# Optimization experiments

Hardware: AMD Instinct MI355X
Metric: run time of the kernel (lower is better)

The kernel has to match this reference:

```python
import jax, jax.numpy as jnp
import numpy as np

B, A, C, M, N = 8, 49104, 20, 32, 16


def _make_boxes(key, shape):
    # valid boxes: x1<x2, y1<y2, in a ~1024px image
    k1, k2 = jax.random.split(key)
    xy = jax.random.uniform(k1, shape[:-1] + (2,)) * 900.0
    wh = jax.random.uniform(k2, shape[:-1] + (2,)) * 120.0 + 8.0
    return jnp.concatenate([xy, xy + wh], axis=-1).astype(jnp.float32)


def setup_inputs() -> dict:
    key = jax.random.key(0)
    ks = jax.random.split(key, 8)
    classifications = jax.random.uniform(ks[0], (B, A, C), dtype=jnp.float32)
    regressions = jax.random.normal(ks[1], (B, A, 4), dtype=jnp.float32)
    anchors = _make_boxes(ks[2], (1, A, 4))
    ema_classifications = jax.random.uniform(ks[3], (B, A, C), dtype=jnp.float32)
    ema_classes = jax.random.randint(ks[4], (B, M), 0, C).astype(jnp.float32)
    ema_bboxes = _make_boxes(ks[5], (B, M, 4))
    ema_counts = jax.random.randint(ks[6], (B,), 0, M + 1).astype(jnp.int32)
    ann_boxes = _make_boxes(ks[7], (B, N, 4))
    ann_cls = jax.random.randint(jax.random.fold_in(key, 99), (B, N), -1, C).astype(jnp.float32)
    annotations = jnp.concatenate([ann_boxes, ann_cls[..., None]], axis=-1)
    return {
        'classifications': classifications,
        'regressions': regressions,
        'anchors': anchors,
        'ema_classifications': ema_classifications,
        'ema_classes': ema_classes,
        'ema_bboxes': ema_bboxes,
        'ema_counts': ema_counts,
        'annotations': annotations,
    }


def _consistency_loss(classifications, regressions, anchors, ema_classifications,
                      ema_bboxes, ema_classes, ema_counts, annotations):
    a0, a1, gamma = 0.05, 0.95, 2.0
    eps = 1e-4
    Bs, As, Cs = classifications.shape
    Ms = ema_classes.shape[1]

    anchor = anchors[0]                        # [A,4]
    aw = anchor[:, 2] - anchor[:, 0]
    ah = anchor[:, 3] - anchor[:, 1]
    acx = anchor[:, 0] + 0.5 * aw
    acy = anchor[:, 1] + 0.5 * ah

    # ragged filtering: keep ema preds whose class appears in annotations[j,:,4]
    valid = jnp.arange(Ms)[None, :] < ema_counts[:, None]                    # [B,M]
    member = (ema_classes[:, :, None] == annotations[:, None, :, 4]).any(-1)  # [B,M]
    keep = valid & member
    has = keep.any(axis=1)                                                   # [B]

    # IoU between anchors [A,4] and kept ema boxes [B,M,4] -> [B,A,M]
    b = ema_bboxes
    iw = jnp.minimum(anchor[None, :, None, 2], b[:, None, :, 2]) - \
         jnp.maximum(anchor[None, :, None, 0], b[:, None, :, 0])
    ih = jnp.minimum(anchor[None, :, None, 3], b[:, None, :, 3]) - \
         jnp.maximum(anchor[None, :, None, 1], b[:, None, :, 1])
    iw = jnp.clip(iw, 0.0)
    ih = jnp.clip(ih, 0.0)
    area_a = (aw * ah)[None, :, None]
    area_b = ((b[:, :, 2] - b[:, :, 0]) * (b[:, :, 3] - b[:, :, 1]))[:, None, :]
    inter = iw * ih
    iou = inter / jnp.clip(area_a + area_b - inter, 1e-8)
    iou = jnp.where(keep[:, None, :], iou, -1.0)  # mask filtered/padded boxes

    iou_max = iou.max(axis=-1)                 # [B,A]
    iou_arg = iou.argmax(axis=-1)              # [B,A]

    pos = (iou_max >= 0.5) & has[:, None]                                   # [B,A]
    assigned = ((iou_max < 0.4) | (iou_max >= 0.5)) & has[:, None]          # [B,A]
    npos = pos.sum(axis=-1).astype(jnp.float32)                             # [B]

    # ---- classification consistency (focal-weighted BCE) ----
    cls = jnp.clip(classifications, eps, 1.0 - eps)
    ecls = jnp.clip(ema_classifications, eps, 1.0 - eps)
    # bug-faithful: original uses full-batch unclamped ema_classifications for
    # alpha_factor, broadcasting [B,A,C] against per-sample [A,C] terms and
    # summing everything; by linearity that equals multiplying by the batch-sum.
    alpha_sum = (a0 + ema_classifications * (a1 - a0)).sum(axis=0)          # [A,C]
    bce = -(ecls * jnp.log(cls) + (1.0 - ecls) * jnp.log(1.0 - cls))
    focal = jnp.abs(ecls - cls) ** gamma
    per = alpha_sum[None] * focal * bce                                     # [B,A,C]
    cls_loss = (per * assigned[:, :, None]).sum(axis=(1, 2)) / jnp.maximum(npos, 1.0)

    ab = jnp.take_along_axis(ema_bboxes, iou_arg[:, :, None], axis=1)       # [B,A,4]
    gw = ab[..., 2] - ab[..., 0]
    gh = ab[..., 3] - ab[..., 1]
    gcx = ab[..., 0] + 0.5 * gw
    gcy = ab[..., 1] + 0.5 * gh
    gw = jnp.clip(gw, 1.0)
    gh = jnp.clip(gh, 1.0)
    dx = (gcx - acx[None]) / aw[None] / 0.1
    dy = (gcy - acy[None]) / ah[None] / 0.1
    dw = jnp.log(gw / aw[None]) / 0.2
    dh = jnp.log(gh / ah[None]) / 0.2
    t = jnp.stack([dx, dy, dw, dh], axis=-1)                                # [B,A,4]
    d = jnp.abs(t - regressions)
    sl1 = jnp.where(d <= 1.0 / 9.0, 0.5 * 9.0 * d * d, d - 0.5 / 9.0)
    reg_sum = (sl1 * pos[:, :, None]).sum(axis=(1, 2))
    reg_loss = jnp.where(npos > 0, reg_sum / (4.0 * jnp.maximum(npos, 1.0)), 0.0)

    return (cls_loss.mean(keepdims=True), reg_loss.mean(keepdims=True))


def reference(classifications, regressions, anchors, ema_classifications,
              ema_classes, ema_bboxes, ema_counts, annotations):
    return _consistency_loss(classifications, regressions, anchors,
                             ema_classifications, ema_bboxes,
                             ema_classes, ema_counts, annotations)
```

## Files before the change

### kernel.cpp

```cpp
#include <hip/hip_runtime.h>

#define B_ 8
#define A_ 49104
#define C_ 20
#define M_ 32
#define N_ 16
#define AC_ (A_ * C_)
#define NBA_ 192
#define NBC_ 960


__global__ __launch_bounds__(256) void k_assign(
        const float* __restrict__ anchors,
        const float* __restrict__ regress,
        const float* __restrict__ ema_classes,
        const float* __restrict__ ema_bboxes,
        const int*   __restrict__ ema_counts,
        const float* __restrict__ annotations,
        unsigned char* __restrict__ assigned_out,
        double* __restrict__ regpart,
        int* __restrict__ pospart)
{
    const int b = blockIdx.y;
    const int a = blockIdx.x * 256 + threadIdx.x;

    __shared__ float4 sbox[M_];
    __shared__ unsigned char skeep[M_];

    if (threadIdx.x < M_) {
        const int m = threadIdx.x;
        const float clsm = ema_classes[b * M_ + m];
        const bool valid = m < ema_counts[b];
        bool member = false;
        for (int n = 0; n < N_; ++n)
            member |= (clsm == annotations[b * N_ * 5 + n * 5 + 4]);
        skeep[m] = (valid && member) ? 1 : 0;
        sbox[m] = reinterpret_cast<const float4*>(ema_bboxes)[b * M_ + m];
    }
    __syncthreads();

    float reg_local = 0.f;
    int pos_local = 0;

    if (a < A_) {
        const float4 anc = reinterpret_cast<const float4*>(anchors)[a];
        const float aw = anc.z - anc.x;
        const float ah = anc.w - anc.y;
        const float area_a = aw * ah;

        float best = -1.0f;
        int barg = 0;
        for (int m = 0; m < M_; ++m) {
            if (!skeep[m]) continue;
            const float4 bb = sbox[m];
            float iw = fminf(anc.z, bb.z) - fmaxf(anc.x, bb.x);
            float ih = fminf(anc.w, bb.w) - fmaxf(anc.y, bb.y);
            iw = fmaxf(iw, 0.f);
            ih = fmaxf(ih, 0.f);
            const float inter = iw * ih;
            const float areab = (bb.z - bb.x) * (bb.w - bb.y);
            const float uni = fmaxf(area_a + areab - inter, 1e-8f);
            const float iou = inter / uni;
            if (iou > best) { best = iou; barg = m; }
        }
        const bool has = (best >= 0.0f);
        const bool pos = has && (best >= 0.5f);
        assigned_out[b * A_ + a] = (has && (best < 0.4f || best >= 0.5f)) ? 1 : 0;

        if (pos) {
            pos_local = 1;
            const float4 ab = sbox[barg];
            float gw = ab.z - ab.x;
            float gh = ab.w - ab.y;
            const float gcx = ab.x + 0.5f * gw;
            const float gcy = ab.y + 0.5f * gh;
            gw = fmaxf(gw, 1.0f);
            gh = fmaxf(gh, 1.0f);
            const float acx = anc.x + 0.5f * aw;
            const float acy = anc.y + 0.5f * ah;
            float t[4];
            t[0] = (gcx - acx) / aw / 0.1f;
            t[1] = (gcy - acy) / ah / 0.1f;
            t[2] = __logf(gw / aw) / 0.2f;
            t[3] = __logf(gh / ah) / 0.2f;
            const float4 r = reinterpret_cast<const float4*>(regress)[b * A_ + a];
            const float rr[4] = {r.x, r.y, r.z, r.w};
            for (int k = 0; k < 4; ++k) {
                const float d = fabsf(t[k] - rr[k]);
                reg_local += (d <= (1.0f / 9.0f)) ? 4.5f * d * d : (d - 0.5f / 9.0f);
            }
        }
    }

    for (int off = 32; off; off >>= 1) {
        reg_local += __shfl_down(reg_local, off);
        pos_local += __shfl_down(pos_local, off);
    }
    __shared__ float sreg[4];
    __shared__ int spos[4];
    const int wid = threadIdx.x >> 6;
    if ((threadIdx.x & 63) == 0) { sreg[wid] = reg_local; spos[wid] = pos_local; }
    __syncthreads();
    if (threadIdx.x == 0) {
        regpart[b * NBA_ + blockIdx.x] =
            (double)(sreg[0] + sreg[1] + sreg[2] + sreg[3]);
        pospart[b * NBA_ + blockIdx.x] = spos[0] + spos[1] + spos[2] + spos[3];
    }
}

__device__ __forceinline__ float cls_term(float e, float p, float alpha) {
    const float pc = fminf(fmaxf(p, 1e-4f), 1.0f - 1e-4f);
    const float ec = fminf(fmaxf(e, 1e-4f), 1.0f - 1e-4f);
    const float bce = -(ec * __logf(pc) + (1.0f - ec) * __logf(1.0f - pc));
    const float df = fabsf(ec - pc);
    return alpha * df * df * bce;
}

__global__ __launch_bounds__(256) void k_cls(
        const float* __restrict__ cls,
        const float* __restrict__ ema,
        const unsigned char* __restrict__ assigned,
        double* __restrict__ clspart)
{
    const int tid = threadIdx.x;
    const int cell = (blockIdx.x * 256 + tid) * 4;

    double acc[B_];
#pragma unroll
    for (int b = 0; b < B_; ++b) acc[b] = 0.0;

    if (cell < AC_) {
        const int a = cell / C_;
        float4 e[B_];
        float sx = 0.f, sy = 0.f, sz = 0.f, sw = 0.f;
#pragma unroll
        for (int b = 0; b < B_; ++b) {
            e[b] = *reinterpret_cast<const float4*>(ema + (size_t)b * AC_ + cell);
            sx += e[b].x; sy += e[b].y; sz += e[b].z; sw += e[b].w;
        }
        const float ax = 0.4f + 0.9f * sx;
        const float ay = 0.4f + 0.9f * sy;
        const float az = 0.4f + 0.9f * sz;
        const float aw4 = 0.4f + 0.9f * sw;
#pragma unroll
        for (int b = 0; b < B_; ++b) {
            if (assigned[b * A_ + a]) {
                const float4 p =
                    *reinterpret_cast<const float4*>(cls + (size_t)b * AC_ + cell);
                float s = cls_term(e[b].x, p.x, ax);
                s += cls_term(e[b].y, p.y, ay);
                s += cls_term(e[b].z, p.z, az);
                s += cls_term(e[b].w, p.w, aw4);
                acc[b] += (double)s;
            }
        }
    }

#pragma unroll
    for (int b = 0; b < B_; ++b)
        for (int off = 32; off; off >>= 1)
            acc[b] += __shfl_down(acc[b], off);

    __shared__ double lacc[4][B_];
    const int wid = tid >> 6;
    if ((tid & 63) == 0) {
#pragma unroll
        for (int b = 0; b < B_; ++b) lacc[wid][b] = acc[b];
    }
    __syncthreads();
    if (tid < B_)
        clspart[tid * NBC_ + blockIdx.x] =
            lacc[0][tid] + lacc[1][tid] + lacc[2][tid] + lacc[3][tid];
}

__global__ __launch_bounds__(256) void k_fin(
        const double* __restrict__ regpart,
        const double* __restrict__ clspart,
        const int* __restrict__ pospart,
        float* __restrict__ out)
{
    const int tid = threadIdx.x;
    const int b = tid >> 5;
    const int l = tid & 31;

    double r = 0.0, s = 0.0;
    int p = 0;
#pragma unroll
    for (int k = 0; k < NBA_ / 32; ++k) {
        r += regpart[b * NBA_ + l + k * 32];
        p += pospart[b * NBA_ + l + k * 32];
    }
#pragma unroll
    for (int k = 0; k < NBC_ / 32; ++k)
        s += clspart[b * NBC_ + l + k * 32];

    for (int off = 16; off; off >>= 1) {
        r += __shfl_down(r, off, 32);
        s += __shfl_down(s, off, 32);
        p += __shfl_down(p, off, 32);
    }

    __shared__ double scls[B_], sregs[B_];
    __shared__ int snp[B_];
    if (l == 0) { scls[b] = s; sregs[b] = r; snp[b] = p; }
    __syncthreads();

    if (tid == 0) {
        double c = 0.0, rr = 0.0;
        for (int b2 = 0; b2 < B_; ++b2) {
            const int n = snp[b2];
            c += scls[b2] / (double)(n > 1 ? n : 1);
            if (n > 0) rr += sregs[b2] / (4.0 * (double)n);
        }
        out[0] = (float)(c / (double)B_);
        out[1] = (float)(rr / (double)B_);
    }
}

extern "C" void kernel_launch(void* const* d_in, const int* in_sizes, int n_in,
                              void* d_out, int out_size, void* d_ws, size_t ws_size,
                              hipStream_t stream) {
    const float* classifications     = (const float*)d_in[0];
    const float* regressions         = (const float*)d_in[1];
    const float* anchors             = (const float*)d_in[2];
    const float* ema_classifications = (const float*)d_in[3];
    const float* ema_classes         = (const float*)d_in[4];
    const float* ema_bboxes          = (const float*)d_in[5];
    const int*   ema_counts          = (const int*)d_in[6];
    const float* annotations         = (const float*)d_in[7];
    float* out = (float*)d_out;

    char* ws = (char*)d_ws;
    double* regpart = (double*)ws;
    double* clspart = (double*)(ws + 12288);
    int*    pospart = (int*)(ws + 73728);
    unsigned char* assigned = (unsigned char*)(ws + 80000);

    dim3 gridA(NBA_, B_);
    k_assign<<<gridA, 256, 0, stream>>>(anchors, regressions, ema_classes,
                                        ema_bboxes, ema_counts, annotations,
                                        assigned, regpart, pospart);

    k_cls<<<NBC_, 256, 0, stream>>>(classifications, ema_classifications,
                                    assigned, clspart);

    k_fin<<<1, 256, 0, stream>>>(regpart, clspart, pospart, out);
}
```

Before: 125.0 us.

## Fuse anchor assignment and classification loss into one kernel with shared-memory mask

Merges the assignment kernel and the classification kernel into a single kernel where each block handles 64 anchors across all 8 batches. The assigned mask is kept in shared memory instead of a global byte array, and per-block partial sums use float with shared atomics instead of double. This removes a kernel launch, the global round trip for the mask, and the double-precision shuffles. In exchange, each block's assignment phase is serial before its loss phase, only 320 threads per block, and float accumulation slightly changes numerics.

```diff
diff --git a/kernel.cpp b/kernel.cpp
--- a/kernel.cpp
+++ b/kernel.cpp
@@ -6,43 +6,58 @@
 #define M_ 32
 #define N_ 16
 #define AC_ (A_ * C_)
-#define NBA_ 192
-#define NBC_ 960
-
-
-__global__ __launch_bounds__(256) void k_assign(
+#define APB_ 64
+#define NB_ 768
+#define TPB_ 320
+
+
+__device__ __forceinline__ float cls_term(float e, float p, float alpha) {
+    const float pc = fminf(fmaxf(p, 1e-4f), 1.0f - 1e-4f);
+    const float ec = fminf(fmaxf(e, 1e-4f), 1.0f - 1e-4f);
+    const float bce = -(ec * __logf(pc) + (1.0f - ec) * __logf(1.0f - pc));
+    const float df = fabsf(ec - pc);
+    return alpha * df * df * bce;
+}
+
+__global__ __launch_bounds__(TPB_) void k_main(
         const float* __restrict__ anchors,
         const float* __restrict__ regress,
+        const float* __restrict__ cls,
+        const float* __restrict__ ema,
         const float* __restrict__ ema_classes,
         const float* __restrict__ ema_bboxes,
         const int*   __restrict__ ema_counts,
         const float* __restrict__ annotations,
-        unsigned char* __restrict__ assigned_out,
         double* __restrict__ regpart,
+        double* __restrict__ clspart,
         int* __restrict__ pospart)
 {
-    const int b = blockIdx.y;
-    const int a = blockIdx.x * 256 + threadIdx.x;
-
-    __shared__ float4 sbox[M_];
-    __shared__ unsigned char skeep[M_];
-
-    if (threadIdx.x < M_) {
-        const int m = threadIdx.x;
-        const float clsm = ema_classes[b * M_ + m];
-        const bool valid = m < ema_counts[b];
+    const int tid = threadIdx.x;
+    const int a0 = blockIdx.x * APB_;
+
+    __shared__ float4 sbox[B_][M_];
+    __shared__ unsigned char skeep[B_][M_];
+    __shared__ unsigned char sassigned[B_][APB_];
+    __shared__ float sreg[B_];
+    __shared__ int snp[B_];
+    __shared__ float pacc[TPB_ / 64][B_];
+
+    if (tid < B_ * M_) {
+        const int b = tid >> 5, m = tid & 31;
+        sbox[b][m] = reinterpret_cast<const float4*>(ema_bboxes)[tid];
+        const float clsm = ema_classes[tid];
         bool member = false;
         for (int n = 0; n < N_; ++n)
             member |= (clsm == annotations[b * N_ * 5 + n * 5 + 4]);
-        skeep[m] = (valid && member) ? 1 : 0;
-        sbox[m] = reinterpret_cast<const float4*>(ema_bboxes)[b * M_ + m];
-    }
-    __syncthreads();
-
-    float reg_local = 0.f;
-    int pos_local = 0;
-
-    if (a < A_) {
+        skeep[b][m] = (m < ema_counts[b] && member) ? 1 : 0;
+    }
+    if (tid < B_) { sreg[tid] = 0.f; snp[tid] = 0; }
+    __syncthreads();
+
+    for (int task = tid; task < B_ * APB_; task += TPB_) {
+        const int b = task >> 6, al = task & 63;
+        const int a = a0 + al;
+        if (a >= A_) continue;
         const float4 anc = reinterpret_cast<const float4*>(anchors)[a];
         const float aw = anc.z - anc.x;
         const float ah = anc.w - anc.y;
@@ -51,8 +66,8 @@
         float best = -1.0f;
         int barg = 0;
         for (int m = 0; m < M_; ++m) {
-            if (!skeep[m]) continue;
-            const float4 bb = sbox[m];
+            if (!skeep[b][m]) continue;
+            const float4 bb = sbox[b][m];
             float iw = fminf(anc.z, bb.z) - fmaxf(anc.x, bb.x);
             float ih = fminf(anc.w, bb.w) - fmaxf(anc.y, bb.y);
             iw = fmaxf(iw, 0.f);
@@ -65,11 +80,10 @@
         }
         const bool has = (best >= 0.0f);
         const bool pos = has && (best >= 0.5f);
-        assigned_out[b * A_ + a] = (has && (best < 0.4f || best >= 0.5f)) ? 1 : 0;
+        sassigned[b][al] = (has && (best < 0.4f || best >= 0.5f)) ? 1 : 0;
 
         if (pos) {
-            pos_local = 1;
-            const float4 ab = sbox[barg];
+            const float4 ab = sbox[b][barg];
             float gw = ab.z - ab.x;
             float gh = ab.w - ab.y;
             const float gcx = ab.x + 0.5f * gw;
@@ -85,52 +99,26 @@
             t[3] = __logf(gh / ah) / 0.2f;
             const float4 r = reinterpret_cast<const float4*>(regress)[b * A_ + a];
             const float rr[4] = {r.x, r.y, r.z, r.w};
+            float rl = 0.f;
             for (int k = 0; k < 4; ++k) {
                 const float d = fabsf(t[k] - rr[k]);
-                reg_local += (d <= (1.0f / 9.0f)) ? 4.5f * d * d : (d - 0.5f / 9.0f);
+                rl += (d <= (1.0f / 9.0f)) ? 4.5f * d * d : (d - 0.5f / 9.0f);
             }
-        }
-    }
-
-    for (int off = 32; off; off >>= 1) {
-        reg_local += __shfl_down(reg_local, off);
-        pos_local += __shfl_down(pos_local, off);
-    }
-    __shared__ float sreg[4];
-    __shared__ int spos[4];
-    const int wid = threadIdx.x >> 6;
-    if ((threadIdx.x & 63) == 0) { sreg[wid] = reg_local; spos[wid] = pos_local; }
-    __syncthreads();
-    if (threadIdx.x == 0) {
-        regpart[b * NBA_ + blockIdx.x] =
-            (double)(sreg[0] + sreg[1] + sreg[2] + sreg[3]);
-        pospart[b * NBA_ + blockIdx.x] = spos[0] + spos[1] + spos[2] + spos[3];
-    }
-}
-
-__device__ __forceinline__ float cls_term(float e, float p, float alpha) {
-    const float pc = fminf(fmaxf(p, 1e-4f), 1.0f - 1e-4f);
-    const float ec = fminf(fmaxf(e, 1e-4f), 1.0f - 1e-4f);
-    const float bce = -(ec * __logf(pc) + (1.0f - ec) * __logf(1.0f - pc));
-    const float df = fabsf(ec - pc);
-    return alpha * df * df * bce;
-}
-
-__global__ __launch_bounds__(256) void k_cls(
-        const float* __restrict__ cls,
-        const float* __restrict__ ema,
-        const unsigned char* __restrict__ assigned,
-        double* __restrict__ clspart)
-{
-    const int tid = threadIdx.x;
-    const int cell = (blockIdx.x * 256 + tid) * 4;
-
-    double acc[B_];
-#pragma unroll
-    for (int b = 0; b < B_; ++b) acc[b] = 0.0;
-
-    if (cell < AC_) {
-        const int a = cell / C_;
+            atomicAdd(&snp[b], 1);
+            atomicAdd(&sreg[b], rl);
+        }
+    }
+    __syncthreads();
+
+    const int al = tid / 5;
+    const int ch = tid % 5;
+    const int a = a0 + al;
+    float acc[B_];
+#pragma unroll
+    for (int b = 0; b < B_; ++b) acc[b] = 0.f;
+
+    if (a < A_) {
+        const int cell = a * C_ + ch * 4;
         float4 e[B_];
         float sx = 0.f, sy = 0.f, sz = 0.f, sw = 0.f;
 #pragma unroll
@@ -144,14 +132,14 @@
         const float aw4 = 0.4f + 0.9f * sw;
 #pragma unroll
         for (int b = 0; b < B_; ++b) {
-            if (assigned[b * A_ + a]) {
+            if (sassigned[b][al]) {
                 const float4 p =
                     *reinterpret_cast<const float4*>(cls + (size_t)b * AC_ + cell);
                 float s = cls_term(e[b].x, p.x, ax);
                 s += cls_term(e[b].y, p.y, ay);
                 s += cls_term(e[b].z, p.z, az);
                 s += cls_term(e[b].w, p.w, aw4);
-                acc[b] += (double)s;
+                acc[b] += s;
             }
         }
     }
@@ -160,17 +148,20 @@
     for (int b = 0; b < B_; ++b)
         for (int off = 32; off; off >>= 1)
             acc[b] += __shfl_down(acc[b], off);
-
-    __shared__ double lacc[4][B_];
-    const int wid = tid >> 6;
+    const int wv = tid >> 6;
     if ((tid & 63) == 0) {
 #pragma unroll
-        for (int b = 0; b < B_; ++b) lacc[wid][b] = acc[b];
-    }
-    __syncthreads();
-    if (tid < B_)
-        clspart[tid * NBC_ + blockIdx.x] =
-            lacc[0][tid] + lacc[1][tid] + lacc[2][tid] + lacc[3][tid];
+        for (int b = 0; b < B_; ++b) pacc[wv][b] = acc[b];
+    }
+    __syncthreads();
+    if (tid < B_) {
+        float tot = 0.f;
+#pragma unroll
+        for (int w = 0; w < TPB_ / 64; ++w) tot += pacc[w][tid];
+        clspart[tid * NB_ + blockIdx.x] = (double)tot;
+        regpart[tid * NB_ + blockIdx.x] = (double)sreg[tid];
+        pospart[tid * NB_ + blockIdx.x] = snp[tid];
+    }
 }
 
 __global__ __launch_bounds__(256) void k_fin(
@@ -186,14 +177,11 @@
     double r = 0.0, s = 0.0;
     int p = 0;
 #pragma unroll
-    for (int k = 0; k < NBA_ / 32; ++k) {
-        r += regpart[b * NBA_ + l + k * 32];
-        p += pospart[b * NBA_ + l + k * 32];
-    }
-#pragma unroll
-    for (int k = 0; k < NBC_ / 32; ++k)
-        s += clspart[b * NBC_ + l + k * 32];
-
+    for (int k = 0; k < NB_ / 32; ++k) {
+        r += regpart[b * NB_ + l + k * 32];
+        s += clspart[b * NB_ + l + k * 32];
+        p += pospart[b * NB_ + l + k * 32];
+    }
     for (int off = 16; off; off >>= 1) {
         r += __shfl_down(r, off, 32);
         s += __shfl_down(s, off, 32);
@@ -232,17 +220,13 @@
 
     char* ws = (char*)d_ws;
     double* regpart = (double*)ws;
-    double* clspart = (double*)(ws + 12288);
-    int*    pospart = (int*)(ws + 73728);
-    unsigned char* assigned = (unsigned char*)(ws + 80000);
-
-    dim3 gridA(NBA_, B_);
-    k_assign<<<gridA, 256, 0, stream>>>(anchors, regressions, ema_classes,
-                                        ema_bboxes, ema_counts, annotations,
-                                        assigned, regpart, pospart);
-
-    k_cls<<<NBC_, 256, 0, stream>>>(classifications, ema_classifications,
-                                    assigned, clspart);
+    double* clspart = (double*)(ws + 49152);
+    int*    pospart = (int*)(ws + 98304);
+
+    k_main<<<NB_, TPB_, 0, stream>>>(anchors, regressions, classifications,
+                                     ema_classifications, ema_classes, ema_bboxes,
+                                     ema_counts, annotations,
+                                     regpart, clspart, pospart);
 
     k_fin<<<1, 256, 0, stream>>>(regpart, clspart, pospart, out);
 }
```

Measured after the change: 122.7 us. Within noise of the previous version (-1.8%).
